# Optimization experiments

Measured on AMD Instinct MI355X. Metric: run time of the kernel, lower is better.

## Reference

```python
import jax, jax.numpy as jnp
import numpy as np

EPS = 1e-7
ROUTINGS = 3


def squash(s, axis=-1):
    # norm over `axis`; faithful to torch: (|s|^2/(1+|s|^2)) * (s/(|s|+eps))
    norm = jnp.linalg.norm(s, axis=axis, keepdims=True)
    sq = norm * norm
    return (sq / (1.0 + sq)) * (s / (norm + EPS))


def conv2d(x, w, b, stride):
    y = jax.lax.conv_general_dilated(
        x, w, window_strides=(stride, stride), padding='VALID',
        dimension_numbers=('NCHW', 'OIHW', 'NCHW'))
    return y + b[None, :, None, None]


def setup_inputs() -> dict:
    key = jax.random.key(0)
    ks = jax.random.split(key, 12)
    B = 256
    return {
        'x': jax.random.normal(ks[0], (B, 1, 28, 28), dtype=jnp.float32),
        'conv1_w': 0.05 * jax.random.normal(ks[1], (256, 1, 9, 9), dtype=jnp.float32),
        'conv1_b': jnp.zeros((256,), jnp.float32),
        'conv2_w': 0.02 * jax.random.normal(ks[2], (256, 256, 9, 9), dtype=jnp.float32),
        'conv2_b': jnp.zeros((256,), jnp.float32),
        'W_caps': 0.01 * jax.random.normal(ks[3], (10, 1152, 16, 8), dtype=jnp.float32),
        'dec_w1': 0.05 * jax.random.normal(ks[4], (160, 512), dtype=jnp.float32),
        'dec_b1': jnp.zeros((512,), jnp.float32),
        'dec_w2': 0.04 * jax.random.normal(ks[5], (512, 1024), dtype=jnp.float32),
        'dec_b2': jnp.zeros((1024,), jnp.float32),
        'dec_w3': 0.03 * jax.random.normal(ks[6], (1024, 784), dtype=jnp.float32),
        'dec_b3': jnp.zeros((784,), jnp.float32),
    }


def reference(x, conv1_w, conv1_b, conv2_w, conv2_b, W_caps,
              dec_w1, dec_b1, dec_w2, dec_b2, dec_w3, dec_b3):
    B = x.shape[0]
    # conv1: [B,1,28,28] -> [B,256,20,20]
    h = conv2d(x, conv1_w, conv1_b, stride=1)
    # primary capsules: conv -> [B,256,6,6]
    h = conv2d(h, conv2_w, conv2_b, stride=2)
    # faithful to original: squash over the LAST spatial axis (dim=-1)
    h = squash(h, axis=-1)
    u = h.reshape(B, -1, 8)  # [B,1152,8]

    # u_hat[b,o,i,d] = W_caps[o,i,d,e] @ u[b,i,e]  -> [B,10,1152,16]
    u_hat = jnp.einsum('oide,bie->boid', W_caps, u)
    u_hat_det = jax.lax.stop_gradient(u_hat)

    b_logits = jnp.zeros((B, 10, 1152), u_hat.dtype)
    for it in range(ROUTINGS):
        c = jax.nn.softmax(b_logits, axis=1)  # over output capsules
        if it == ROUTINGS - 1:
            v = squash(jnp.sum(c[:, :, :, None] * u_hat, axis=-2, keepdims=True))
        else:
            v = squash(jnp.sum(c[:, :, :, None] * u_hat_det, axis=-2, keepdims=True))
            b_logits = b_logits + jnp.sum(v * u_hat_det, axis=-1)
    v = jnp.squeeze(v, axis=-2)  # [B,10,16]

    length = jnp.linalg.norm(v, axis=-1)  # [B,10]
    # y defaults to one-hot of argmax(length), constant w.r.t. grads
    y = jax.lax.stop_gradient(
        jax.nn.one_hot(jnp.argmax(length, axis=1), 10, dtype=v.dtype))
    masked = (v * y[:, :, None]).reshape(B, -1)  # [B,160]
    h1 = jax.nn.relu(masked @ dec_w1 + dec_b1)
    h2 = jax.nn.relu(h1 @ dec_w2 + dec_b2)
    reconstruction = jax.nn.sigmoid(h2 @ dec_w3 + dec_b3)  # [B,784]
    return length, reconstruction
```

## Files before the change

kernel.cpp:

```cpp
#include <hip/hip_runtime.h>
#include <cstdint>
#include <cstddef>

typedef __bf16 bf16x8 __attribute__((ext_vector_type(8)));
typedef float  floatx4 __attribute__((ext_vector_type(4)));
typedef float  floatx2 __attribute__((ext_vector_type(2)));
typedef float  floatx16 __attribute__((ext_vector_type(16)));
typedef int    intx4v __attribute__((ext_vector_type(4)));
typedef int    intx8 __attribute__((ext_vector_type(8)));
typedef unsigned short ushort8 __attribute__((ext_vector_type(8)));
typedef unsigned short ushort4v __attribute__((ext_vector_type(4)));

__device__ __forceinline__ float bflo(unsigned int u) {
    union { unsigned int u32; float f; } x; x.u32 = u << 16; return x.f;
}
__device__ __forceinline__ float bfhi(unsigned int u) {
    union { unsigned int u32; float f; } x; x.u32 = u & 0xffff0000u; return x.f;
}
__device__ __forceinline__ unsigned short f2bf(float f) {
    union { float f; unsigned int u; } x; x.f = f;
    unsigned int u = x.u;
    unsigned int r = (u + 0x7fffu + ((u >> 16) & 1u)) >> 16;
    return (unsigned short)r;
}
__device__ __forceinline__ unsigned char f2fp8(float f) {
    unsigned int pk = __builtin_amdgcn_cvt_pk_fp8_f32(f, f, 0, false);
    return (unsigned char)(pk & 0xff);
}
__device__ __forceinline__ void fp8x4_dec(unsigned int u, float* f) {
    floatx2 lo = __builtin_amdgcn_cvt_pk_f32_fp8(u, false);
    floatx2 hi = __builtin_amdgcn_cvt_pk_f32_fp8(u, true);
    f[0] = lo[0]; f[1] = lo[1]; f[2] = hi[0]; f[3] = hi[1];
}

#define GLOBAL_U32 const __attribute__((address_space(1))) unsigned int*
#define LDS_U32 __attribute__((address_space(3))) unsigned int*
__device__ __forceinline__ void async_cp16(const void* g, void* l) {
    __builtin_amdgcn_global_load_lds((GLOBAL_U32)g, (LDS_U32)l, 16, 0, 0);
}

#define UHAT_SCALE 64.0f
#define UHAT_INV   (1.0f / 64.0f)
#define W2_SCALE   16.0f
#define W2_INV     (1.0f / 16.0f)

__global__ __launch_bounds__(256) void prep_k(const float* __restrict__ x,
                                              const float* __restrict__ w1c,
                                              const float* __restrict__ b1c,
                                              const float* __restrict__ w2,
                                              unsigned char* __restrict__ h1t8,
                                              unsigned char* __restrict__ w2t8,
                                              float* __restrict__ S012) {
    const int blk = blockIdx.x, t = threadIdx.x;
    if (t < 120) S012[blk * 120 + t] = 0.f;
    __shared__ float shm[10368];
    if (blk < 512) {
        const int b = blk >> 1, hh = blk & 1;
        const int oh0 = hh * 10;
        for (int idx = t; idx < 504; idx += 256) shm[idx] = x[b * 784 + oh0 * 28 + idx];
        __syncthreads();
        const float* wr = w1c + t * 81;
        const float bv = b1c[t];
        for (int ohl = 0; ohl < 10; ++ohl) {
            float acc[20];
#pragma unroll
            for (int ow = 0; ow < 20; ++ow) acc[ow] = bv;
#pragma unroll
            for (int kh = 0; kh < 9; ++kh) {
                float xr[28];
                const float* xrow = &shm[(ohl + kh) * 28];
#pragma unroll
                for (int q = 0; q < 7; ++q) *(float4*)&xr[q * 4] = *(const float4*)&xrow[q * 4];
#pragma unroll
                for (int kw = 0; kw < 9; ++kw) {
                    const float wv = wr[kh * 9 + kw];
#pragma unroll
                    for (int ow = 0; ow < 20; ++ow) acc[ow] = fmaf(xr[ow + kw], wv, acc[ow]);
                }
            }
            unsigned char* orow = h1t8 + (size_t)((b * 20 + oh0 + ohl) * 20) * 256 + t;
#pragma unroll
            for (int ow = 0; ow < 20; ++ow) orow[ow * 256] = f2fp8(acc[ow]);
        }
    } else {
        const int id = blk - 512;
        const int oc = id >> 1, half = id & 1;
        const float* src = w2 + (size_t)oc * 20736 + half * 128 * 81;
        for (int idx = t; idx < 10368; idx += 256) shm[idx] = src[idx];
        __syncthreads();
        unsigned char* dst = w2t8 + (size_t)oc * 20736 + half * 128;
        for (int idx = t; idx < 10368; idx += 256) {
            const int tap = idx >> 7, icl = idx & 127;
            dst[tap * 256 + icl] = f2fp8(shm[icl * 81 + tap] * W2_SCALE);
        }
    }
}

__device__ __forceinline__ int c2_rowbase(int m) {
    const int b = m / 36, sp = m % 36;
    const int oh = sp / 6, ow = sp % 6;
    return (b * 400 + oh * 40 + ow * 2) * 256;
}

__global__ __launch_bounds__(256) void conv2_k(const unsigned char* __restrict__ h1t8,
                                               const unsigned char* __restrict__ w2t8,
                                               unsigned short* __restrict__ part) {
    const int t = threadIdx.x;
    const int id = blockIdx.x;
    const int G = id >> 4;
    const int bx = (id >> 3) & 1;
    const int s = id & 7;
    const int by = 2 * G + (s >> 2);
    const int z  = ((s & 3) + by) & 3;
    __shared__ unsigned char At[128 * 128];
    __shared__ unsigned char Bt[128 * 128];

    const int oc0 = bx * 128;

    int aRB[4], bBase[4];
#pragma unroll
    for (int k = 0; k < 4; ++k) {
        const int a = t + 256 * k;
        const int r = a >> 3, sg = a & 7;
        const int u = sg ^ (r & 7);
        aRB[k] = c2_rowbase(by * 128 + r) + u * 16;
        bBase[k] = (oc0 + r) * 20736 + u * 16;
    }

    const int lane = t & 63, l31 = lane & 31, h = lane >> 5;
    const int wave = t >> 6;
    const int wM = (wave & 1) * 64, wOC = (wave >> 1) * 64;

    int aO[2][2][2], bO[2][2][2];
#pragma unroll
    for (int i = 0; i < 2; ++i) {
        const int Ra = wOC + i * 32 + l31;
        const int Rb = wM + i * 32 + l31;
#pragma unroll
        for (int st = 0; st < 2; ++st)
#pragma unroll
            for (int p = 0; p < 2; ++p) {
                const int c = st * 4 + h * 2 + p;
                aO[st][i][p] = Ra * 128 + ((c ^ (Ra & 7)) << 4);
                bO[st][i][p] = Rb * 128 + ((c ^ (Rb & 7)) << 4);
            }
    }

    floatx16 acc[2][2];
#pragma unroll
    for (int i = 0; i < 2; ++i)
#pragma unroll
        for (int j = 0; j < 2; ++j)
#pragma unroll
            for (int r = 0; r < 16; ++r) acc[i][j][r] = 0.f;

    const int q0 = (162 * z) >> 2, q1 = (162 * (z + 1)) >> 2;
    for (int q = q0; q < q1; ++q) {
        const int tap = q >> 1;
        const int kh = tap / 9, kw = tap - 9 * kh;
        const int aoffB = (kh * 20 + kw) * 256 + (q & 1) * 128;
        __syncthreads();
#pragma unroll
        for (int k = 0; k < 4; ++k)
            async_cp16(h1t8 + aRB[k] + aoffB, At + (t + 256 * k) * 16);
#pragma unroll
        for (int k = 0; k < 4; ++k)
            async_cp16(w2t8 + bBase[k] + q * 128, Bt + (t + 256 * k) * 16);
        __syncthreads();
#pragma unroll
        for (int st = 0; st < 2; ++st) {
            intx8 aF[2], bF[2];
#pragma unroll
            for (int i = 0; i < 2; ++i) {
                const intx4v alo = *(const intx4v*)(Bt + aO[st][i][0]);
                const intx4v ahi = *(const intx4v*)(Bt + aO[st][i][1]);
                aF[i] = (intx8){alo[0], alo[1], alo[2], alo[3], ahi[0], ahi[1], ahi[2], ahi[3]};
                const intx4v blo = *(const intx4v*)(At + bO[st][i][0]);
                const intx4v bhi = *(const intx4v*)(At + bO[st][i][1]);
                bF[i] = (intx8){blo[0], blo[1], blo[2], blo[3], bhi[0], bhi[1], bhi[2], bhi[3]};
            }
#pragma unroll
            for (int i = 0; i < 2; ++i)
#pragma unroll
                for (int j = 0; j < 2; ++j)
                    acc[i][j] = __builtin_amdgcn_mfma_scale_f32_32x32x64_f8f6f4(
                        aF[i], bF[j], acc[i][j], 0, 0, 0, 127, 0, 127);
        }
    }

    unsigned short* pz = part + (size_t)z * 2359296;
#pragma unroll
    for (int i = 0; i < 2; ++i) {
#pragma unroll
        for (int j = 0; j < 2; ++j) {
            const int m = by * 128 + wM + j * 32 + l31;
#pragma unroll
            for (int rg = 0; rg < 4; ++rg) {
                const int oc = oc0 + wOC + i * 32 + rg * 8 + 4 * h;
                ushort4v pk;
#pragma unroll
                for (int rr = 0; rr < 4; ++rr) pk[rr] = f2bf(acc[i][j][rg * 4 + rr] * W2_INV);
                *(ushort4v*)(pz + (size_t)m * 256 + oc) = pk;
            }
        }
    }
}

__global__ __launch_bounds__(256) void squash_u_k(const unsigned short* __restrict__ part,
                                                  const float* __restrict__ bias,
                                                  float* __restrict__ u) {
    const int bb = blockIdx.x, t = threadIdx.x;
    const int b = bb >> 1, h = bb & 1;
    __shared__ float hs[4608];
    const size_t base = (size_t)b * 9216 + h * 4608;
    for (int q = t; q < 2304; q += 256) {
        const int idx = q * 2;
        float v0 = bias[idx & 255], v1 = bias[(idx + 1) & 255];
#pragma unroll
        for (int z = 0; z < 4; ++z) {
            const unsigned int uu = *(const unsigned int*)(part + (size_t)z * 2359296 + base + idx);
            v0 += bflo(uu);
            v1 += bfhi(uu);
        }
        hs[idx] = v0; hs[idx + 1] = v1;
    }
    __syncthreads();
    for (int gq = t; gq < 768; gq += 256) {
        const int c = gq / 3, ohl = gq % 3;
        const int oh = h * 3 + ohl;
        float s[6], sq = 0.f;
#pragma unroll
        for (int ow = 0; ow < 6; ++ow) { s[ow] = hs[(ohl * 6 + ow) * 256 + c]; sq = fmaf(s[ow], s[ow], sq); }
        const float norm = sqrtf(sq);
        const float f = (sq / (1.0f + sq)) / (norm + 1e-7f);
        float* up = u + (size_t)b * 9216 + c * 36 + oh * 6;
#pragma unroll
        for (int ow = 0; ow < 6; ++ow) up[ow] = s[ow] * f;
    }
}

__global__ __launch_bounds__(256) void uhat_k(const float* __restrict__ Wc,
                                              const float* __restrict__ u,
                                              unsigned int* __restrict__ uhat8) {
    const int i = blockIdx.x, t = threadIdx.x;
    __shared__ float Wl[1280];
    for (int idx = t; idx < 1280; idx += 256) {
        const int o = idx >> 7, r = idx & 127;
        Wl[idx] = Wc[((size_t)o * 1152 + i) * 128 + r];
    }
    float ur[8];
    *(float4*)&ur[0] = *(const float4*)(u + (size_t)t * 9216 + i * 8);
    *(float4*)&ur[4] = *(const float4*)(u + (size_t)t * 9216 + i * 8 + 4);
    __syncthreads();
    unsigned int* row = uhat8 + ((size_t)i * 256 + t) * 40;
#pragma unroll 1
    for (int o = 0; o < 10; ++o) {
        float vals[16];
#pragma unroll
        for (int d = 0; d < 16; ++d) {
            const float* wp = &Wl[o * 128 + d * 8];
            float a = 0.f;
#pragma unroll
            for (int e = 0; e < 8; ++e) a = fmaf(wp[e], ur[e], a);
            vals[d] = a * UHAT_SCALE;
        }
        uint4 pk;
        unsigned int w;
#pragma unroll
        for (int q = 0; q < 4; ++q) {
            w = 0;
            w = __builtin_amdgcn_cvt_pk_fp8_f32(vals[q * 4 + 0], vals[q * 4 + 1], w, false);
            w = __builtin_amdgcn_cvt_pk_fp8_f32(vals[q * 4 + 2], vals[q * 4 + 3], w, true);
            if (q == 0) pk.x = w; else if (q == 1) pk.y = w; else if (q == 2) pk.z = w; else pk.w = w;
        }
        *(uint4*)(row + o * 4) = pk;
    }
}

__global__ __launch_bounds__(256) void route_iter0_k(const unsigned int* __restrict__ uhat8,
                                                     float* __restrict__ S0) {
    const int b = blockIdx.x, i0 = blockIdx.y * 128, t = threadIdx.x;
    __shared__ __align__(16) unsigned int Ul8[128 * 40];
    const unsigned int* ub = uhat8 + ((size_t)i0 * 256 + b) * 40;
#pragma unroll
    for (int rep = 0; rep < 5; ++rep) {
        const int c = rep * 256 + t;
        const int row = c / 10, q = c - row * 10;
        async_cp16(ub + (size_t)row * 10240 + q * 4, (char*)Ul8 + c * 16);
    }
    __syncthreads();
    const int th = t & 127, hi = t >> 7;
    if (th < 40) {
        const unsigned int* p = Ul8 + hi * 64 * 40 + th;
        float a0 = 0.f, a1 = 0.f, a2 = 0.f, a3 = 0.f;
#pragma unroll 4
        for (int i = 0; i < 64; ++i) {
            float f[4];
            fp8x4_dec(p[i * 40], f);
            a0 += f[0]; a1 += f[1]; a2 += f[2]; a3 += f[3];
        }
        const float sc = 0.1f * UHAT_INV;
        atomicAdd(&S0[b * 160 + 4 * th + 0], sc * a0);
        atomicAdd(&S0[b * 160 + 4 * th + 1], sc * a1);
        atomicAdd(&S0[b * 160 + 4 * th + 2], sc * a2);
        atomicAdd(&S0[b * 160 + 4 * th + 3], sc * a3);
    }
}

template <int ITER>
__global__ __launch_bounds__(256) void route_iter_k(const unsigned int* __restrict__ uhat8,
                                                    const float* __restrict__ S_in,
                                                    float* __restrict__ BL,
                                                    float* __restrict__ S_out) {
    const int b = blockIdx.x, i0 = blockIdx.y * 128, t = threadIdx.x;
    __shared__ __align__(16) unsigned int Ul8[128 * 40];
    __shared__ float Vl[160];
    __shared__ float cT[10 * 132];
    __shared__ float dots[128 * 10];

    const unsigned int* ub = uhat8 + ((size_t)i0 * 256 + b) * 40;
#pragma unroll
    for (int rep = 0; rep < 5; ++rep) {
        const int c = rep * 256 + t;
        const int row = c / 10, q = c - row * 10;
        async_cp16(ub + (size_t)row * 10240 + q * 4, (char*)Ul8 + c * 16);
    }

    if (t < 160) {
        const float x = S_in[b * 160 + t];
        float sq = x * x;
        sq += __shfl_xor(sq, 1, 16);
        sq += __shfl_xor(sq, 2, 16);
        sq += __shfl_xor(sq, 4, 16);
        sq += __shfl_xor(sq, 8, 16);
        const float norm = sqrtf(sq);
        const float f = (sq / (1.f + sq)) / (norm + 1e-7f);
        Vl[t] = x * f;
    }
    __syncthreads();

    const int o = t % 10, s = t / 10;
    float vr[16];
    if (t < 250) {
#pragma unroll
        for (int q = 0; q < 4; ++q)
            *(float4*)&vr[q * 4] = *(const float4*)(&Vl[o * 16 + q * 4]);
    }

    if (t < 250) {
#pragma unroll
        for (int rep = 0; rep < 6; ++rep) {
            const int i = s + 25 * rep;
            if (i < 128) {
                const uint4 uu = *(const uint4*)(Ul8 + i * 40 + o * 4);
                float f[16];
                fp8x4_dec(uu.x, f);
                fp8x4_dec(uu.y, f + 4);
                fp8x4_dec(uu.z, f + 8);
                fp8x4_dec(uu.w, f + 12);
                float dot = 0.f;
#pragma unroll
                for (int d = 0; d < 16; ++d) dot = fmaf(f[d], vr[d], dot);
                dots[i * 10 + o] = dot * UHAT_INV;
            }
        }
    }
    __syncthreads();

    if (t < 128) {
        float bl[10];
#pragma unroll
        for (int oo = 0; oo < 10; ++oo) bl[oo] = dots[t * 10 + oo];
        if (ITER == 2) {
#pragma unroll
            for (int oo = 0; oo < 10; ++oo) bl[oo] += BL[(size_t)b * 11520 + oo * 1152 + i0 + t];
        } else {
#pragma unroll
            for (int oo = 0; oo < 10; ++oo) BL[(size_t)b * 11520 + oo * 1152 + i0 + t] = bl[oo];
        }
        float mx = bl[0];
#pragma unroll
        for (int oo = 1; oo < 10; ++oo) mx = fmaxf(mx, bl[oo]);
        float ex[10], sum = 0.f;
#pragma unroll
        for (int oo = 0; oo < 10; ++oo) { ex[oo] = expf(bl[oo] - mx); sum += ex[oo]; }
        const float inv = 1.f / sum;
#pragma unroll
        for (int oo = 0; oo < 10; ++oo) cT[oo * 132 + t] = ex[oo] * inv;
    }
    __syncthreads();

    const int th = t & 127, hi = t >> 7;
    if (th < 40) {
        const int oq = th >> 2;
        const unsigned int* base = Ul8 + hi * 64 * 40 + th;
        const float* cb = &cT[oq * 132 + hi * 64];
        float a0 = 0.f, a1 = 0.f, a2 = 0.f, a3 = 0.f;
#pragma unroll 4
        for (int ii = 0; ii < 64; ++ii) {
            const float c = cb[ii];
            float f[4];
            fp8x4_dec(base[ii * 40], f);
            a0 = fmaf(c, f[0], a0);
            a1 = fmaf(c, f[1], a1);
            a2 = fmaf(c, f[2], a2);
            a3 = fmaf(c, f[3], a3);
        }
        atomicAdd(&S_out[b * 160 + 4 * th + 0], a0 * UHAT_INV);
        atomicAdd(&S_out[b * 160 + 4 * th + 1], a1 * UHAT_INV);
        atomicAdd(&S_out[b * 160 + 4 * th + 2], a2 * UHAT_INV);
        atomicAdd(&S_out[b * 160 + 4 * th + 3], a3 * UHAT_INV);
    }
}

__global__ __launch_bounds__(512) void final_k(const float* __restrict__ S,
                                               const float* __restrict__ w1,
                                               const float* __restrict__ b1,
                                               float* __restrict__ out_len,
                                               float* __restrict__ h1d) {
    const int b = blockIdx.x, t = threadIdx.x;
    __shared__ float v_s[160];
    __shared__ float len_s[10];
    __shared__ int sel_s;
    if (t < 160) {
        const float x = S[b * 160 + t];
        float sq = x * x;
        sq += __shfl_xor(sq, 1, 16);
        sq += __shfl_xor(sq, 2, 16);
        sq += __shfl_xor(sq, 4, 16);
        sq += __shfl_xor(sq, 8, 16);
        const float norm = sqrtf(sq);
        const float f = (sq / (1.f + sq)) / (norm + 1e-7f);
        v_s[t] = x * f;
        if ((t & 15) == 0) {
            const float len = f * norm;
            len_s[t >> 4] = len;
            out_len[b * 10 + (t >> 4)] = len;
        }
    }
    __syncthreads();
    if (t == 0) {
        float best = len_s[0]; int bi = 0;
        for (int oo = 1; oo < 10; ++oo) if (len_s[oo] > best) { best = len_s[oo]; bi = oo; }
        sel_s = bi;
    }
    __syncthreads();
    const int s = sel_s;
    float acc = b1[t];
    const float* wrow = w1 + (size_t)(s * 16) * 512 + t;
#pragma unroll
    for (int j = 0; j < 16; ++j) acc = fmaf(v_s[s * 16 + j], wrow[j * 512], acc);
    h1d[(size_t)b * 512 + t] = fmaxf(acc, 0.f);
}

template <int ACT>
__global__ __launch_bounds__(256) void mlp3_k(const float* __restrict__ A,
                                              const float* __restrict__ Bm,
                                              const float* __restrict__ bias,
                                              float* __restrict__ C, int N, int K) {
    extern __shared__ float Asm[];
    const int t = threadIdx.x;
    const int m0 = blockIdx.y * 8, n0 = blockIdx.x * 64;
    const int RS = K + 4;
    const int k4 = K >> 2;
    for (int i = t; i < 8 * k4; i += 256) {
        const int r = i / k4, c = i - r * k4;
        *(float4*)&Asm[r * RS + c * 4] = *(const float4*)&A[(size_t)(m0 + r) * K + c * 4];
    }
    __syncthreads();
    const int lane = t & 63, w = t >> 6;
    const int mq = lane >> 4, nq = lane & 15;
    const int n = n0 + nq * 4;
    const int ncl = (n + 3 < N) ? n : (N - 4);
    const float* bp = Bm + ncl;
    const float* asA = &Asm[(mq * 2 + 0) * RS];
    const float* asB = &Asm[(mq * 2 + 1) * RS];
    const int kQ = K >> 2;
    const int kBeg = w * kQ;
    const int nBat2 = kQ >> 4;
    float4 acc0 = {0.f, 0.f, 0.f, 0.f}, acc1 = {0.f, 0.f, 0.f, 0.f};
    float4 ba[8], bb[8];
#pragma unroll
    for (int d = 0; d < 8; ++d) ba[d] = *(const float4*)&bp[(size_t)(kBeg + d) * N];

#define MLP3_FMA(BATCH, KB)                                                       \
    _Pragma("unroll")                                                             \
    for (int d = 0; d < 8; ++d) {                                                 \
        const float4 b = BATCH[d];                                                \
        const float a0 = asA[(KB) + d];                                           \
        const float a1 = asB[(KB) + d];                                           \
        acc0.x = fmaf(a0, b.x, acc0.x); acc0.y = fmaf(a0, b.y, acc0.y);           \
        acc0.z = fmaf(a0, b.z, acc0.z); acc0.w = fmaf(a0, b.w, acc0.w);           \
        acc1.x = fmaf(a1, b.x, acc1.x); acc1.y = fmaf(a1, b.y, acc1.y);           \
        acc1.z = fmaf(a1, b.z, acc1.z); acc1.w = fmaf(a1, b.w, acc1.w);           \
    }

    int k = kBeg;
#pragma unroll 1
    for (int it = 0; it < nBat2; ++it) {
#pragma unroll
        for (int d = 0; d < 8; ++d) bb[d] = *(const float4*)&bp[(size_t)(k + 8 + d) * N];
        MLP3_FMA(ba, k)
        if (it + 1 < nBat2) {
#pragma unroll
            for (int d = 0; d < 8; ++d) ba[d] = *(const float4*)&bp[(size_t)(k + 16 + d) * N];
        }
        MLP3_FMA(bb, k + 8)
        k += 16;
    }
#undef MLP3_FMA

    __syncthreads();
    float* red = Asm;
    float* my = &red[(size_t)(w * 64 + lane) * 8];
    my[0] = acc0.x; my[1] = acc0.y; my[2] = acc0.z; my[3] = acc0.w;
    my[4] = acc1.x; my[5] = acc1.y; my[6] = acc1.z; my[7] = acc1.w;
    __syncthreads();
    if (t < 64) {
        float o[8];
#pragma unroll
        for (int x = 0; x < 8; ++x)
            o[x] = red[(size_t)t * 8 + x] + red[(size_t)(64 + t) * 8 + x]
                 + red[(size_t)(128 + t) * 8 + x] + red[(size_t)(192 + t) * 8 + x];
        const int nn = n0 + (t & 15) * 4;
#pragma unroll
        for (int rm = 0; rm < 2; ++rm) {
            const int m = m0 + (t >> 4) * 2 + rm;
#pragma unroll
            for (int rn = 0; rn < 4; ++rn) {
                const int ncol = nn + rn;
                if (ncol < N) {
                    float v = o[rm * 4 + rn] + bias[ncol];
                    if (ACT == 0) v = fmaxf(v, 0.f);
                    else v = 1.f / (1.f + expf(-v));
                    C[(size_t)m * N + ncol] = v;
                }
            }
        }
    }
}

extern "C" void kernel_launch(void* const* d_in, const int* in_sizes, int n_in,
                              void* d_out, int out_size, void* d_ws, size_t ws_size,
                              hipStream_t stream) {
    const float* x   = (const float*)d_in[0];
    const float* w1  = (const float*)d_in[1];
    const float* b1  = (const float*)d_in[2];
    const float* w2  = (const float*)d_in[3];
    const float* b2  = (const float*)d_in[4];
    const float* Wc  = (const float*)d_in[5];
    const float* dw1 = (const float*)d_in[6];
    const float* db1 = (const float*)d_in[7];
    const float* dw2 = (const float*)d_in[8];
    const float* db2 = (const float*)d_in[9];
    const float* dw3 = (const float*)d_in[10];
    const float* db3 = (const float*)d_in[11];
    float* out = (float*)d_out;

    char* ws = (char*)d_ws;
    unsigned char* H1T8 = (unsigned char*)(ws + 0);
    unsigned char* W2T8 = (unsigned char*)(ws + 26214400);
    unsigned short* PART = (unsigned short*)(ws + 31522816);
    unsigned int*   UHAT = (unsigned int*)(ws + 0);
    float* U    = (float*)(ws + 50397184);
    float* BL   = (float*)(ws + 59834368);
    float* S012 = (float*)(ws + 71630848);
    float* H1D  = (float*)(ws + 59834368);
    float* H2D  = (float*)(ws + 60358656);

    float* S0 = S012, *S1 = S012 + 40960, *S2 = S012 + 81920;

    prep_k<<<1024, 256, 0, stream>>>(x, w1, b1, w2, H1T8, W2T8, S012);
    conv2_k<<<576, 256, 0, stream>>>(H1T8, W2T8, PART);
    squash_u_k<<<512, 256, 0, stream>>>(PART, b2, U);
    uhat_k<<<1152, 256, 0, stream>>>(Wc, U, UHAT);
    route_iter0_k<<<dim3(256, 9), 256, 0, stream>>>(UHAT, S0);
    route_iter_k<1><<<dim3(256, 9), 256, 0, stream>>>(UHAT, S0, BL, S1);
    route_iter_k<2><<<dim3(256, 9), 256, 0, stream>>>(UHAT, S1, BL, S2);
    final_k<<<256, 512, 0, stream>>>(S2, dw1, db1, out, H1D);
    mlp3_k<0><<<dim3(16, 32), 256, 8 * 516 * 4, stream>>>(H1D, dw2, db2, H2D, 1024, 512);
    mlp3_k<1><<<dim3(13, 32), 256, 8 * 1028 * 4, stream>>>(H2D, dw3, db3, out + 2560, 784, 1024);
}
```

Measured before the change: 350.5 us.

## Compute conv1 with bf16 MFMA instead of scalar FMA loops

Rewrites the conv1 portion of the prep kernel as an implicit GEMM on matrix cores. Each block handles one image and 128 channels: weights are converted to bf16 in LDS and padded from 81 to 96 taps, and input patches are gathered into bf16 fragments for mfma_f32_16x16x32_bf16. Outputs are packed four at a time into fp8 stores. This removes the per-thread scalar FMA work, at the cost of bf16 rounding of inputs and weights and an irregular gather from LDS.

```diff
diff --git a/kernel.cpp b/kernel.cpp
--- a/kernel.cpp
+++ b/kernel.cpp
@@ -3,6 +3,7 @@
 #include <cstddef>
 
 typedef __bf16 bf16x8 __attribute__((ext_vector_type(8)));
+typedef short  shortx8 __attribute__((ext_vector_type(8)));
 typedef float  floatx4 __attribute__((ext_vector_type(4)));
 typedef float  floatx2 __attribute__((ext_vector_type(2)));
 typedef float  floatx16 __attribute__((ext_vector_type(16)));
@@ -53,36 +54,76 @@
                                               float* __restrict__ S012) {
     const int blk = blockIdx.x, t = threadIdx.x;
     if (t < 120) S012[blk * 120 + t] = 0.f;
-    __shared__ float shm[10368];
     if (blk < 512) {
-        const int b = blk >> 1, hh = blk & 1;
-        const int oh0 = hh * 10;
-        for (int idx = t; idx < 504; idx += 256) shm[idx] = x[b * 784 + oh0 * 28 + idx];
+        __shared__ float xs[1024];
+        __shared__ unsigned short wb[96 * 132];
+        const int b = blk >> 1, ch0 = (blk & 1) * 128;
+        for (int i = t; i < 1024; i += 256) xs[i] = (i < 784) ? x[b * 784 + i] : 0.f;
+        for (int i = t; i < 96 * 132; i += 256) wb[i] = 0;
         __syncthreads();
-        const float* wr = w1c + t * 81;
-        const float bv = b1c[t];
-        for (int ohl = 0; ohl < 10; ++ohl) {
-            float acc[20];
-#pragma unroll
-            for (int ow = 0; ow < 20; ++ow) acc[ow] = bv;
-#pragma unroll
-            for (int kh = 0; kh < 9; ++kh) {
-                float xr[28];
-                const float* xrow = &shm[(ohl + kh) * 28];
-#pragma unroll
-                for (int q = 0; q < 7; ++q) *(float4*)&xr[q * 4] = *(const float4*)&xrow[q * 4];
-#pragma unroll
-                for (int kw = 0; kw < 9; ++kw) {
-                    const float wv = wr[kh * 9 + kw];
-#pragma unroll
-                    for (int ow = 0; ow < 20; ++ow) acc[ow] = fmaf(xr[ow + kw], wv, acc[ow]);
+        for (int i = t; i < 81 * 128; i += 256) {
+            const int tap = i >> 7, chl = i & 127;
+            wb[tap * 132 + chl] = f2bf(w1c[(size_t)(ch0 + chl) * 81 + tap]);
+        }
+        __syncthreads();
+        const int lane = t & 63, l15 = lane & 15, g = lane >> 4;
+        const int wave = t >> 6;
+        const int n0l = wave * 32;
+        int xoff[3][8];
+#pragma unroll
+        for (int kk = 0; kk < 3; ++kk)
+#pragma unroll
+            for (int e = 0; e < 8; ++e) {
+                const int tap = kk * 32 + g * 8 + e;
+                const int kh = tap / 9, kw = tap - 9 * kh;
+                xoff[kk][e] = kh * 28 + kw;
+            }
+        shortx8 bF[2][3];
+#pragma unroll
+        for (int nt = 0; nt < 2; ++nt)
+#pragma unroll
+            for (int kk = 0; kk < 3; ++kk) {
+                shortx8 v;
+#pragma unroll
+                for (int e = 0; e < 8; ++e) {
+                    const int tap = kk * 32 + g * 8 + e;
+                    v[e] = (short)wb[tap * 132 + n0l + nt * 16 + l15];
                 }
-            }
-            unsigned char* orow = h1t8 + (size_t)((b * 20 + oh0 + ohl) * 20) * 256 + t;
-#pragma unroll
-            for (int ow = 0; ow < 20; ++ow) orow[ow * 256] = f2fp8(acc[ow]);
+                bF[nt][kk] = v;
+            }
+        float bv[2][4];
+#pragma unroll
+        for (int nt = 0; nt < 2; ++nt)
+#pragma unroll
+            for (int r = 0; r < 4; ++r)
+                bv[nt][r] = b1c[ch0 + n0l + nt * 16 + g * 4 + r];
+        for (int mt = 0; mt < 25; ++mt) {
+            const int s = mt * 16 + l15;
+            const int oh = s / 20, ow = s - 20 * oh;
+            const int s2 = oh * 28 + ow;
+            shortx8 aF[3];
+#pragma unroll
+            for (int kk = 0; kk < 3; ++kk) {
+                shortx8 v;
+#pragma unroll
+                for (int e = 0; e < 8; ++e) v[e] = (short)f2bf(xs[s2 + xoff[kk][e]]);
+                aF[kk] = v;
+            }
+            const size_t sbase = ((size_t)(b * 20 + oh) * 20 + ow) * 256 + ch0 + n0l + g * 4;
+#pragma unroll
+            for (int nt = 0; nt < 2; ++nt) {
+                floatx4 acc = (floatx4){0.f, 0.f, 0.f, 0.f};
+#pragma unroll
+                for (int kk = 0; kk < 3; ++kk)
+                    acc = __builtin_amdgcn_mfma_f32_16x16x32_bf16(bF[nt][kk], aF[kk], acc, 0, 0, 0);
+                unsigned int w = 0;
+                w = __builtin_amdgcn_cvt_pk_fp8_f32(acc[0] + bv[nt][0], acc[1] + bv[nt][1], w, false);
+                w = __builtin_amdgcn_cvt_pk_fp8_f32(acc[2] + bv[nt][2], acc[3] + bv[nt][3], w, true);
+                *(unsigned int*)(h1t8 + sbase + nt * 16) = w;
+            }
         }
     } else {
+        __shared__ float shm[10368];
         const int id = blk - 512;
         const int oc = id >> 1, half = id & 1;
         const float* src = w2 + (size_t)oc * 20736 + half * 128 * 81;
```

Result: faster. 329.7 us (-5.9%).
